# Kernel optimization log

Hardware: AMD Instinct MI355X
Metric: run time of the kernel (lower is better)

The kernel has to match this reference:

```python
import jax, jax.numpy as jnp
import numpy as np

NUM_ITERATIONS = 5
EPSILON_0 = 1.0
EPS = 1e-20


def setup_inputs() -> dict:
    key = jax.random.key(0)
    k1, k2 = jax.random.split(key)
    B, NIN, NOUT = 8192, 3072, 512
    x = jax.random.uniform(k1, (B, NIN), dtype=jnp.float32)
    w = jax.random.uniform(k2, (NOUT, NIN), dtype=jnp.float32)
    # weights setter normalizes rows to sum to 1
    w = w / w.sum(axis=1, keepdims=True)
    h_initial = jnp.full((NOUT,), 1.0 / NOUT, dtype=jnp.float32)
    return {"x": x, "weights": w, "h_initial": h_initial}


def reference(x, weights, h_initial):
    # x: [B, NIN], weights: [NOUT, NIN], h_initial: [NOUT]
    x = x / (x.sum(axis=1, keepdims=True) + EPS)  # input normalization in forward()
    B = x.shape[0]
    h = jnp.broadcast_to(h_initial[None, :], (B, h_initial.shape[0]))

    def step(h, _):
        # Original: h_w = h[:,:,None]*W[None]; h_w /= h_w.sum(1,keepdim)+eps;
        #           h_w = (h_w * x[:,None,:]).sum(-1)
        # Equivalent without materializing [B, NOUT, NIN]:
        denom = h @ weights                       # [B, NIN] = sum_n h_bn W_nk
        h_w = h * ((x / (denom + EPS)) @ weights.T)  # [B, NOUT]
        h_new = h + EPSILON_0 * h_w               # epsilon_0 > 0 branch
        h_new = h_new / (h_new.sum(axis=1, keepdims=True) + EPS)
        return h_new, None

    h, _ = jax.lax.scan(step, h, None, length=NUM_ITERATIONS)
    return h
```

## Files before the change

kernel.cpp:

```cpp
#include <hip/hip_runtime.h>


#define NIN 3072
#define NOUT 512

using f32x4 = __attribute__((ext_vector_type(4))) float;
using i32x8 = __attribute__((ext_vector_type(8))) int;

union frag32 { i32x8 v; uint4 q[2]; };

#define MFMA128(A, B, C) \
    __builtin_amdgcn_mfma_scale_f32_16x16x128_f8f6f4( \
        (A), (B), (C), 0, 0, 0, (int)0x7f7f7f7f, 0, (int)0x7f7f7f7f)

__device__ __forceinline__ unsigned short f2bf(float f) {
    unsigned int u = __builtin_bit_cast(unsigned int, f);
    return (unsigned short)((u + 0x7fffu + ((u >> 16) & 1u)) >> 16);
}
__device__ __forceinline__ float bf2f(unsigned short s) {
    unsigned int u = ((unsigned int)s) << 16;
    return __builtin_bit_cast(float, u);
}

#define LDS_BARRIER() do {                                   \
    asm volatile("s_waitcnt lgkmcnt(0)" ::: "memory");       \
    __builtin_amdgcn_s_barrier();                            \
    asm volatile("" ::: "memory");                           \
} while (0)

__global__ void prep_all(const float* __restrict__ x,
                         const float* __restrict__ W,
                         const float* __restrict__ h_init,
                         unsigned short* __restrict__ X2,
                         unsigned char* __restrict__ W1,
                         unsigned char* __restrict__ W2,
                         float* __restrict__ d0inv) {
    __shared__ float wsum[4];
    __shared__ float dred[8][32];
    const int bb = blockIdx.x;
    const int t  = threadIdx.x;

    if (bb < 8192) {
        const int b = bb;
        const float4* r4 = reinterpret_cast<const float4*>(x + (size_t)b * NIN);
        float s = 0.f;
        float4 v0 = r4[t], v1 = r4[t + 256], v2 = r4[t + 512];
        s = v0.x + v0.y + v0.z + v0.w + v1.x + v1.y + v1.z + v1.w + v2.x + v2.y + v2.z + v2.w;
        #pragma unroll
        for (int off = 32; off > 0; off >>= 1) s += __shfl_down(s, off, 64);
        int w = t >> 6, l = t & 63;
        if (l == 0) wsum[w] = s;
        __syncthreads();
        float inv = 16.0f / (wsum[0] + wsum[1] + wsum[2] + wsum[3] + 1e-20f);
        unsigned short* orow = X2 + (size_t)b * NIN;
        #pragma unroll
        for (int c = 0; c < 3; ++c) {
            float4 v = (c == 0) ? v0 : (c == 1) ? v1 : v2;
            ushort4 o;
            o.x = f2bf(v.x * inv); o.y = f2bf(v.y * inv);
            o.z = f2bf(v.z * inv); o.w = f2bf(v.w * inv);
            *reinterpret_cast<ushort4*>(orow + (t + c * 256) * 4) = o;
        }
    } else if (bb < 8192 + 384) {
        int tt = (bb - 8192) * 256 + t;
        unsigned int words[8];
        if (tt < 49152) {
            int l = tt & 63, g = tt >> 6;
            int s = g >> 5, rem = g & 31, w = rem >> 2, nt = rem & 3;
            int n = w * 64 + nt * 16 + (l & 15);
            int kbase = s * 128 + ((l >> 4) << 5);
            const float* src = W + (size_t)n * NIN + kbase;
            #pragma unroll
            for (int q = 0; q < 8; ++q) {
                float v0 = src[q * 4 + 0] * 4096.0f, v1 = src[q * 4 + 1] * 4096.0f;
                float v2 = src[q * 4 + 2] * 4096.0f, v3 = src[q * 4 + 3] * 4096.0f;
                int pk = __builtin_amdgcn_cvt_pk_fp8_f32(v0, v1, 0, false);
                pk     = __builtin_amdgcn_cvt_pk_fp8_f32(v2, v3, pk, true);
                words[q] = (unsigned int)pk;
            }
            uint4* dst = reinterpret_cast<uint4*>(W2 + (size_t)tt * 32);
            dst[0] = *reinterpret_cast<uint4*>(&words[0]);
            dst[1] = *reinterpret_cast<uint4*>(&words[4]);
        } else {
            int u = tt - 49152;
            int l = u & 63, g = u >> 6;
            int c = g & 3, sw = g >> 2;
            int w = sw & 7, s = sw >> 3;
            int kout = s * 128 + w * 16 + (l & 15);
            int nbase = c * 128 + ((l >> 4) << 5);
            #pragma unroll
            for (int q = 0; q < 8; ++q) {
                float v0 = W[(size_t)(nbase + q * 4 + 0) * NIN + kout] * 4096.0f;
                float v1 = W[(size_t)(nbase + q * 4 + 1) * NIN + kout] * 4096.0f;
                float v2 = W[(size_t)(nbase + q * 4 + 2) * NIN + kout] * 4096.0f;
                float v3 = W[(size_t)(nbase + q * 4 + 3) * NIN + kout] * 4096.0f;
                int pk = __builtin_amdgcn_cvt_pk_fp8_f32(v0, v1, 0, false);
                pk     = __builtin_amdgcn_cvt_pk_fp8_f32(v2, v3, pk, true);
                words[q] = (unsigned int)pk;
            }
            uint4* dst = reinterpret_cast<uint4*>(W1 + (size_t)u * 32);
            dst[0] = *reinterpret_cast<uint4*>(&words[0]);
            dst[1] = *reinterpret_cast<uint4*>(&words[4]);
        }
    } else {
        int kb = bb - 8576;
        int kid = t & 31, nsub = t >> 5;
        int k = kb * 32 + kid;
        int n0 = nsub * 64;
        float s = 0.f;
        const float* p = W + (size_t)n0 * NIN + k;
        #pragma unroll 8
        for (int n = 0; n < 64; ++n) s += h_init[n0 + n] * p[(size_t)n * NIN];
        dred[nsub][kid] = s;
        __syncthreads();
        if (t < 32) {
            float sm = 1e-20f;
            #pragma unroll
            for (int j = 0; j < 8; ++j) sm += dred[j][t];
            d0inv[kb * 32 + t] = 1.0f / sm;
        }
    }
}

__global__ __launch_bounds__(512, 1) void nnmf_main(
    const unsigned short* __restrict__ X2,
    const unsigned char* __restrict__ W1,
    const unsigned char* __restrict__ W2,
    const float* __restrict__ d0inv,
    const float* __restrict__ h_init,
    float* __restrict__ out)
{
    __shared__ unsigned char  h8_lds[32 * 528];
    __shared__ float          h32_lds[32 * 516];
    __shared__ unsigned short x_lds[32 * 136];
    __shared__ unsigned char  r8_lds[32 * 144];
    __shared__ float red[8][32];

    const int tid = threadIdx.x;
    const int w  = tid >> 6;
    const int l  = tid & 63;
    const int lo = l & 15;
    const int hi = l >> 4;
    const int b0 = blockIdx.x * 32;

    for (int idx = tid; idx < 32 * 512; idx += 512) {
        int r = idx >> 9, c = idx & 511;
        h32_lds[r * 516 + c] = h_init[c];
    }

    const int xrow = tid >> 4, xcc = tid & 15;
    const uint4* xg = reinterpret_cast<const uint4*>(X2 + (size_t)(b0 + xrow) * NIN + xcc * 8);
    unsigned short* xdst = &x_lds[xrow * 136 + xcc * 8];

    const unsigned char* w1base = W1 + (size_t)w * 8192 + (size_t)l * 32;
    const unsigned char* w2base = W2 + (size_t)w * 8192 + (size_t)l * 32;

    *reinterpret_cast<uint4*>(xdst) = xg[0];
    uint4 xnext = xg[16];
    frag32 w1buf[4];
    __syncthreads();

    const float DSCL = 9.5367431640625e-07f;
    const float TS   = 1.0f / 65536.0f;
    f32x4 tacc[2][4];

    for (int it = 0; it < 5; ++it) {
        #pragma unroll
        for (int m = 0; m < 2; ++m)
            #pragma unroll
            for (int nt = 0; nt < 4; ++nt)
                tacc[m][nt] = (f32x4){0.f, 0.f, 0.f, 0.f};

        for (int s = 0; s < 24; ++s) {
            const int sn  = (s + 1 == 24) ? 0 : s + 1;
            const int sn2 = (s + 2 >= 24) ? (s + 2 - 24) : s + 2;

            frag32 w2v[4];
            {
                const unsigned char* w2p = w2base + (size_t)s * 65536;
                #pragma unroll
                for (int nt = 0; nt < 4; ++nt) {
                    const uint4* p = reinterpret_cast<const uint4*>(w2p + nt * 2048);
                    w2v[nt].q[0] = p[0];
                    w2v[nt].q[1] = p[1];
                }
            }

            f32x4 d0 = {0,0,0,0}, d1 = {0,0,0,0};
            float dv = 0.f;
            if (it == 0) {
                dv = d0inv[s * 128 + w * 16 + lo];
            } else {
                #pragma unroll
                for (int c = 0; c < 4; ++c) {
                    frag32 ha0, ha1;
                    const uint4* p0 = reinterpret_cast<const uint4*>(
                        &h8_lds[lo * 528 + c * 128 + hi * 32]);
                    const uint4* p1 = reinterpret_cast<const uint4*>(
                        &h8_lds[(16 + lo) * 528 + c * 128 + hi * 32]);
                    ha0.q[0] = p0[0]; ha0.q[1] = p0[1];
                    ha1.q[0] = p1[0]; ha1.q[1] = p1[1];
                    d0 = MFMA128(ha0.v, w1buf[c].v, d0);
                    d1 = MFMA128(ha1.v, w1buf[c].v, d1);
                }
            }

            #pragma unroll
            for (int i = 0; i < 4; ++i) {
                int row0 = hi * 4 + i;
                float x0 = bf2f(x_lds[row0 * 136 + w * 16 + lo]);
                float x1 = bf2f(x_lds[(16 + row0) * 136 + w * 16 + lo]);
                float r0, r1;
                if (it == 0) { r0 = x0 * dv; r1 = x1 * dv; }
                else {
                    r0 = x0 * __builtin_amdgcn_rcpf(fmaf(d0[i], DSCL, 1e-20f));
                    r1 = x1 * __builtin_amdgcn_rcpf(fmaf(d1[i], DSCL, 1e-20f));
                }
                int c0 = __builtin_amdgcn_cvt_pk_fp8_f32(r0, r0, 0, false);
                int c1 = __builtin_amdgcn_cvt_pk_fp8_f32(r1, r1, 0, false);
                r8_lds[row0 * 144 + w * 16 + lo] = (unsigned char)(c0 & 0xff);
                r8_lds[(16 + row0) * 144 + w * 16 + lo] = (unsigned char)(c1 & 0xff);
            }
            LDS_BARRIER();

            frag32 ra0, ra1;
            {
                const uint4* p0 = reinterpret_cast<const uint4*>(&r8_lds[lo * 144 + hi * 32]);
                const uint4* p1 = reinterpret_cast<const uint4*>(&r8_lds[(16 + lo) * 144 + hi * 32]);
                ra0.q[0] = p0[0]; ra0.q[1] = p0[1];
                ra1.q[0] = p1[0]; ra1.q[1] = p1[1];
            }
            #pragma unroll
            for (int nt = 0; nt < 2; ++nt) {
                tacc[0][nt] = MFMA128(ra0.v, w2v[nt].v, tacc[0][nt]);
                tacc[1][nt] = MFMA128(ra1.v, w2v[nt].v, tacc[1][nt]);
            }

            if (it > 0 || s == 23) {
                const unsigned char* w1p = w1base + (size_t)sn * 65536;
                #pragma unroll
                for (int c = 0; c < 4; ++c) {
                    const uint4* p = reinterpret_cast<const uint4*>(w1p + c * 2048);
                    w1buf[c].q[0] = p[0];
                    w1buf[c].q[1] = p[1];
                }
            }

            #pragma unroll
            for (int nt = 2; nt < 4; ++nt) {
                tacc[0][nt] = MFMA128(ra0.v, w2v[nt].v, tacc[0][nt]);
                tacc[1][nt] = MFMA128(ra1.v, w2v[nt].v, tacc[1][nt]);
            }

            *reinterpret_cast<uint4*>(xdst) = xnext;
            xnext = xg[(size_t)sn2 * 16];
            LDS_BARRIER();
        }

        float hv_[2][4][4];
        float p[2][4];
        #pragma unroll
        for (int m = 0; m < 2; ++m)
            #pragma unroll
            for (int i = 0; i < 4; ++i) p[m][i] = 0.f;

        #pragma unroll
        for (int m = 0; m < 2; ++m)
            #pragma unroll
            for (int nt = 0; nt < 4; ++nt)
                #pragma unroll
                for (int i = 0; i < 4; ++i) {
                    int row = m * 16 + hi * 4 + i;
                    int col = w * 64 + nt * 16 + lo;
                    float hv = h32_lds[row * 516 + col];
                    float v = hv * (1.f + tacc[m][nt][i] * TS);
                    hv_[m][nt][i] = v;
                    p[m][i] += v;
                }
        #pragma unroll
        for (int mask = 1; mask < 16; mask <<= 1)
            #pragma unroll
            for (int m = 0; m < 2; ++m)
                #pragma unroll
                for (int i = 0; i < 4; ++i)
                    p[m][i] += __shfl_xor(p[m][i], mask, 64);
        if (lo == 0) {
            #pragma unroll
            for (int m = 0; m < 2; ++m)
                #pragma unroll
                for (int i = 0; i < 4; ++i)
                    red[w][m * 16 + hi * 4 + i] = p[m][i];
        }
        __syncthreads();
        float inv[2][4];
        #pragma unroll
        for (int m = 0; m < 2; ++m)
            #pragma unroll
            for (int i = 0; i < 4; ++i) {
                int row = m * 16 + hi * 4 + i;
                float S = 0.f;
                #pragma unroll
                for (int ww = 0; ww < 8; ++ww) S += red[ww][row];
                inv[m][i] = 1.f / (S + 1e-20f);
            }

        if (it < 4) {
            #pragma unroll
            for (int m = 0; m < 2; ++m)
                #pragma unroll
                for (int nt = 0; nt < 4; ++nt)
                    #pragma unroll
                    for (int i = 0; i < 4; ++i) {
                        int row = m * 16 + hi * 4 + i;
                        int col = w * 64 + nt * 16 + lo;
                        float hv = hv_[m][nt][i] * inv[m][i];
                        h32_lds[row * 516 + col] = hv;
                        int c = __builtin_amdgcn_cvt_pk_fp8_f32(hv * 256.0f, hv * 256.0f, 0, false);
                        h8_lds[row * 528 + col] = (unsigned char)(c & 0xff);
                    }
            __syncthreads();
        } else {
            #pragma unroll
            for (int m = 0; m < 2; ++m)
                #pragma unroll
                for (int nt = 0; nt < 4; ++nt)
                    #pragma unroll
                    for (int i = 0; i < 4; ++i) {
                        int row = m * 16 + hi * 4 + i;
                        int col = w * 64 + nt * 16 + lo;
                        out[(size_t)(b0 + row) * 512 + col] = hv_[m][nt][i] * inv[m][i];
                    }
        }
    }
}

extern "C" void kernel_launch(void* const* d_in, const int* in_sizes, int n_in,
                              void* d_out, int out_size, void* d_ws, size_t ws_size,
                              hipStream_t stream) {
    const float* x   = (const float*)d_in[0];
    const float* wgt = (const float*)d_in[1];
    const float* h0  = (const float*)d_in[2];
    float* out = (float*)d_out;

    unsigned short* X2 = (unsigned short*)d_ws;
    unsigned char*  W1 = (unsigned char*)((char*)d_ws + 50331648);
    unsigned char*  W2 = (unsigned char*)((char*)d_ws + 51904512);
    float* d0inv       = (float*)((char*)d_ws + 53477376);

    prep_all<<<8672, 256, 0, stream>>>(x, wgt, h0, X2, W1, W2, d0inv);
    nnmf_main<<<256, 512, 0, stream>>>(X2, W1, W2, d0inv, h0, out);
}
```

Measured before the change: 391.2 us.

## Double the K step per iteration to halve barriers and reuse h fragments

Widens the k-chunk processed per loop iteration from 128 to 256 columns, so each iteration runs 12 steps instead of 24. W1 and W2 are repacked in fp8 to match the new per-wave 32-column layout, and the x and r LDS tiles are widened to match. Each loaded h fragment now feeds two MFMAs, and the number of LDS barriers per iteration is halved. In exchange the kernel holds more weight fragments in registers and uses more LDS, which raises register pressure and could cause spills at 512 threads per block.

```diff
diff --git a/kernel.cpp b/kernel.cpp
--- a/kernel.cpp
+++ b/kernel.cpp
@@ -66,9 +66,11 @@
         unsigned int words[8];
         if (tt < 49152) {
             int l = tt & 63, g = tt >> 6;
-            int s = g >> 5, rem = g & 31, w = rem >> 2, nt = rem & 3;
+            int khalf = g & 1, q2 = g >> 1;
+            int nt = q2 & 3, q3 = q2 >> 2;
+            int w = q3 & 7, s = q3 >> 3;
             int n = w * 64 + nt * 16 + (l & 15);
-            int kbase = s * 128 + ((l >> 4) << 5);
+            int kbase = s * 256 + khalf * 128 + ((l >> 4) << 5);
             const float* src = W + (size_t)n * NIN + kbase;
             #pragma unroll
             for (int q = 0; q < 8; ++q) {
@@ -84,9 +86,10 @@
         } else {
             int u = tt - 49152;
             int l = u & 63, g = u >> 6;
-            int c = g & 3, sw = g >> 2;
-            int w = sw & 7, s = sw >> 3;
-            int kout = s * 128 + w * 16 + (l & 15);
+            int kt = g & 1, q2 = g >> 1;
+            int c = q2 & 3, q3 = q2 >> 2;
+            int w = q3 & 7, s = q3 >> 3;
+            int kout = s * 256 + w * 32 + kt * 16 + (l & 15);
             int nbase = c * 128 + ((l >> 4) << 5);
             #pragma unroll
             for (int q = 0; q < 8; ++q) {
@@ -132,8 +135,8 @@
 {
     __shared__ unsigned char  h8_lds[32 * 528];
     __shared__ float          h32_lds[32 * 516];
-    __shared__ unsigned short x_lds[32 * 136];
-    __shared__ unsigned char  r8_lds[32 * 144];
+    __shared__ unsigned short x_lds[32 * 264];
+    __shared__ unsigned char  r8_lds[32 * 272];
     __shared__ float red[8][32];
 
     const int tid = threadIdx.x;
@@ -149,15 +152,17 @@
     }
 
     const int xrow = tid >> 4, xcc = tid & 15;
-    const uint4* xg = reinterpret_cast<const uint4*>(X2 + (size_t)(b0 + xrow) * NIN + xcc * 8);
-    unsigned short* xdst = &x_lds[xrow * 136 + xcc * 8];
-
-    const unsigned char* w1base = W1 + (size_t)w * 8192 + (size_t)l * 32;
-    const unsigned char* w2base = W2 + (size_t)w * 8192 + (size_t)l * 32;
-
-    *reinterpret_cast<uint4*>(xdst) = xg[0];
-    uint4 xnext = xg[16];
-    frag32 w1buf[4];
+    const uint4* xgq = reinterpret_cast<const uint4*>(X2 + (size_t)(b0 + xrow) * NIN);
+    unsigned short* xdst0 = &x_lds[xrow * 264 + xcc * 8];
+    unsigned short* xdst1 = &x_lds[xrow * 264 + 128 + xcc * 8];
+
+    const unsigned char* w1base = W1 + (size_t)w * 16384 + (size_t)l * 32;
+    const unsigned char* w2base = W2 + (size_t)w * 16384 + (size_t)l * 32;
+
+    *reinterpret_cast<uint4*>(xdst0) = xgq[xcc];
+    *reinterpret_cast<uint4*>(xdst1) = xgq[xcc + 16];
+    uint4 xnA = xgq[32 + xcc], xnB = xgq[32 + xcc + 16];
+    frag32 w1w[6];
     __syncthreads();
 
     const float DSCL = 9.5367431640625e-07f;
@@ -171,89 +176,157 @@
             for (int nt = 0; nt < 4; ++nt)
                 tacc[m][nt] = (f32x4){0.f, 0.f, 0.f, 0.f};
 
-        for (int s = 0; s < 24; ++s) {
-            const int sn  = (s + 1 == 24) ? 0 : s + 1;
-            const int sn2 = (s + 2 >= 24) ? (s + 2 - 24) : s + 2;
-
-            frag32 w2v[4];
-            {
-                const unsigned char* w2p = w2base + (size_t)s * 65536;
-                #pragma unroll
-                for (int nt = 0; nt < 4; ++nt) {
-                    const uint4* p = reinterpret_cast<const uint4*>(w2p + nt * 2048);
-                    w2v[nt].q[0] = p[0];
-                    w2v[nt].q[1] = p[1];
-                }
-            }
-
-            f32x4 d0 = {0,0,0,0}, d1 = {0,0,0,0};
-            float dv = 0.f;
+        for (int s = 0; s < 12; ++s) {
+            const unsigned char* w1s = w1base + (size_t)s * 131072;
+            const unsigned char* w2s = w2base + (size_t)s * 131072;
+
+            f32x4 d00 = {0,0,0,0}, d01 = {0,0,0,0}, d10 = {0,0,0,0}, d11 = {0,0,0,0};
+            float dv0 = 0.f, dv1 = 0.f;
             if (it == 0) {
-                dv = d0inv[s * 128 + w * 16 + lo];
+                dv0 = d0inv[s * 256 + w * 32 + lo];
+                dv1 = d0inv[s * 256 + w * 32 + 16 + lo];
             } else {
-                #pragma unroll
-                for (int c = 0; c < 4; ++c) {
-                    frag32 ha0, ha1;
-                    const uint4* p0 = reinterpret_cast<const uint4*>(
-                        &h8_lds[lo * 528 + c * 128 + hi * 32]);
-                    const uint4* p1 = reinterpret_cast<const uint4*>(
-                        &h8_lds[(16 + lo) * 528 + c * 128 + hi * 32]);
+                frag32 ha0, ha1;
+                {
+                    const uint4* p0 = reinterpret_cast<const uint4*>(&h8_lds[lo * 528 + 0 * 128 + hi * 32]);
+                    const uint4* p1 = reinterpret_cast<const uint4*>(&h8_lds[(16 + lo) * 528 + 0 * 128 + hi * 32]);
                     ha0.q[0] = p0[0]; ha0.q[1] = p0[1];
                     ha1.q[0] = p1[0]; ha1.q[1] = p1[1];
-                    d0 = MFMA128(ha0.v, w1buf[c].v, d0);
-                    d1 = MFMA128(ha1.v, w1buf[c].v, d1);
-                }
-            }
-
-            #pragma unroll
-            for (int i = 0; i < 4; ++i) {
-                int row0 = hi * 4 + i;
-                float x0 = bf2f(x_lds[row0 * 136 + w * 16 + lo]);
-                float x1 = bf2f(x_lds[(16 + row0) * 136 + w * 16 + lo]);
-                float r0, r1;
-                if (it == 0) { r0 = x0 * dv; r1 = x1 * dv; }
-                else {
-                    r0 = x0 * __builtin_amdgcn_rcpf(fmaf(d0[i], DSCL, 1e-20f));
-                    r1 = x1 * __builtin_amdgcn_rcpf(fmaf(d1[i], DSCL, 1e-20f));
-                }
-                int c0 = __builtin_amdgcn_cvt_pk_fp8_f32(r0, r0, 0, false);
-                int c1 = __builtin_amdgcn_cvt_pk_fp8_f32(r1, r1, 0, false);
-                r8_lds[row0 * 144 + w * 16 + lo] = (unsigned char)(c0 & 0xff);
-                r8_lds[(16 + row0) * 144 + w * 16 + lo] = (unsigned char)(c1 & 0xff);
+                    d00 = MFMA128(ha0.v, w1w[0].v, d00);
+                    d01 = MFMA128(ha0.v, w1w[1].v, d01);
+                    d10 = MFMA128(ha1.v, w1w[0].v, d10);
+                    d11 = MFMA128(ha1.v, w1w[1].v, d11);
+                }
+                {
+                    const uint4* pa = reinterpret_cast<const uint4*>(w1s + 4 * 2048);
+                    const uint4* pb = reinterpret_cast<const uint4*>(w1s + 5 * 2048);
+                    w1w[4].q[0] = pa[0]; w1w[4].q[1] = pa[1];
+                    w1w[5].q[0] = pb[0]; w1w[5].q[1] = pb[1];
+                }
+                {
+                    const uint4* p0 = reinterpret_cast<const uint4*>(&h8_lds[lo * 528 + 1 * 128 + hi * 32]);
+                    const uint4* p1 = reinterpret_cast<const uint4*>(&h8_lds[(16 + lo) * 528 + 1 * 128 + hi * 32]);
+                    ha0.q[0] = p0[0]; ha0.q[1] = p0[1];
+                    ha1.q[0] = p1[0]; ha1.q[1] = p1[1];
+                    d00 = MFMA128(ha0.v, w1w[2].v, d00);
+                    d01 = MFMA128(ha0.v, w1w[3].v, d01);
+                    d10 = MFMA128(ha1.v, w1w[2].v, d10);
+                    d11 = MFMA128(ha1.v, w1w[3].v, d11);
+                }
+                {
+                    const uint4* pa = reinterpret_cast<const uint4*>(w1s + 6 * 2048);
+                    const uint4* pb = reinterpret_cast<const uint4*>(w1s + 7 * 2048);
+                    w1w[0].q[0] = pa[0]; w1w[0].q[1] = pa[1];
+                    w1w[1].q[0] = pb[0]; w1w[1].q[1] = pb[1];
+                }
+                {
+                    const uint4* p0 = reinterpret_cast<const uint4*>(&h8_lds[lo * 528 + 2 * 128 + hi * 32]);
+                    const uint4* p1 = reinterpret_cast<const uint4*>(&h8_lds[(16 + lo) * 528 + 2 * 128 + hi * 32]);
+                    ha0.q[0] = p0[0]; ha0.q[1] = p0[1];
+                    ha1.q[0] = p1[0]; ha1.q[1] = p1[1];
+                    d00 = MFMA128(ha0.v, w1w[4].v, d00);
+                    d01 = MFMA128(ha0.v, w1w[5].v, d01);
+                    d10 = MFMA128(ha1.v, w1w[4].v, d10);
+                    d11 = MFMA128(ha1.v, w1w[5].v, d11);
+                }
+                {
+                    const uint4* p0 = reinterpret_cast<const uint4*>(&h8_lds[lo * 528 + 3 * 128 + hi * 32]);
+                    const uint4* p1 = reinterpret_cast<const uint4*>(&h8_lds[(16 + lo) * 528 + 3 * 128 + hi * 32]);
+                    ha0.q[0] = p0[0]; ha0.q[1] = p0[1];
+                    ha1.q[0] = p1[0]; ha1.q[1] = p1[1];
+                    d00 = MFMA128(ha0.v, w1w[0].v, d00);
+                    d01 = MFMA128(ha0.v, w1w[1].v, d01);
+                    d10 = MFMA128(ha1.v, w1w[0].v, d10);
+                    d11 = MFMA128(ha1.v, w1w[1].v, d11);
+                }
+            }
+
+            frag32 w2a[4];
+            #pragma unroll
+            for (int nt = 0; nt < 4; ++nt) {
+                const uint4* p = reinterpret_cast<const uint4*>(w2s + (nt * 2) * 2048);
+                w2a[nt].q[0] = p[0];
+                w2a[nt].q[1] = p[1];
+            }
+
+            #pragma unroll
+            for (int kt = 0; kt < 2; ++kt) {
+                int col = w * 32 + kt * 16 + lo;
+                #pragma unroll
+                for (int i = 0; i < 4; ++i) {
+                    int row0 = hi * 4 + i;
+                    float x0 = bf2f(x_lds[row0 * 264 + col]);
+                    float x1 = bf2f(x_lds[(16 + row0) * 264 + col]);
+                    float r0, r1;
+                    if (it == 0) {
+                        float dvv = kt ? dv1 : dv0;
+                        r0 = x0 * dvv; r1 = x1 * dvv;
+                    } else {
+                        float e0 = kt ? d01[i] : d00[i];
+                        float e1 = kt ? d11[i] : d10[i];
+                        r0 = x0 * __builtin_amdgcn_rcpf(fmaf(e0, DSCL, 1e-20f));
+                        r1 = x1 * __builtin_amdgcn_rcpf(fmaf(e1, DSCL, 1e-20f));
+                    }
+                    int c0 = __builtin_amdgcn_cvt_pk_fp8_f32(r0, r0, 0, false);
+                    int c1 = __builtin_amdgcn_cvt_pk_fp8_f32(r1, r1, 0, false);
+                    r8_lds[row0 * 272 + col] = (unsigned char)(c0 & 0xff);
+                    r8_lds[(16 + row0) * 272 + col] = (unsigned char)(c1 & 0xff);
+                }
             }
             LDS_BARRIER();
 
-            frag32 ra0, ra1;
+            frag32 w2b[4];
+            #pragma unroll
+            for (int nt = 0; nt < 4; ++nt) {
+                const uint4* p = reinterpret_cast<const uint4*>(w2s + (nt * 2 + 1) * 2048);
+                w2b[nt].q[0] = p[0];
+                w2b[nt].q[1] = p[1];
+            }
+
             {
-                const uint4* p0 = reinterpret_cast<const uint4*>(&r8_lds[lo * 144 + hi * 32]);
-                const uint4* p1 = reinterpret_cast<const uint4*>(&r8_lds[(16 + lo) * 144 + hi * 32]);
+                frag32 ra0, ra1;
+                const uint4* p0 = reinterpret_cast<const uint4*>(&r8_lds[lo * 272 + hi * 32]);
+                const uint4* p1 = reinterpret_cast<const uint4*>(&r8_lds[(16 + lo) * 272 + hi * 32]);
                 ra0.q[0] = p0[0]; ra0.q[1] = p0[1];
                 ra1.q[0] = p1[0]; ra1.q[1] = p1[1];
-            }
-            #pragma unroll
-            for (int nt = 0; nt < 2; ++nt) {
-                tacc[0][nt] = MFMA128(ra0.v, w2v[nt].v, tacc[0][nt]);
-                tacc[1][nt] = MFMA128(ra1.v, w2v[nt].v, tacc[1][nt]);
-            }
-
-            if (it > 0 || s == 23) {
-                const unsigned char* w1p = w1base + (size_t)sn * 65536;
-                #pragma unroll
-                for (int c = 0; c < 4; ++c) {
-                    const uint4* p = reinterpret_cast<const uint4*>(w1p + c * 2048);
-                    w1buf[c].q[0] = p[0];
-                    w1buf[c].q[1] = p[1];
-                }
-            }
-
-            #pragma unroll
-            for (int nt = 2; nt < 4; ++nt) {
-                tacc[0][nt] = MFMA128(ra0.v, w2v[nt].v, tacc[0][nt]);
-                tacc[1][nt] = MFMA128(ra1.v, w2v[nt].v, tacc[1][nt]);
-            }
-
-            *reinterpret_cast<uint4*>(xdst) = xnext;
-            xnext = xg[(size_t)sn2 * 16];
+                #pragma unroll
+                for (int nt = 0; nt < 4; ++nt) {
+                    tacc[0][nt] = MFMA128(ra0.v, w2a[nt].v, tacc[0][nt]);
+                    tacc[1][nt] = MFMA128(ra1.v, w2a[nt].v, tacc[1][nt]);
+                }
+            }
+
+            if (it > 0 || s == 11) {
+                int sw = (s == 11) ? 0 : s + 1;
+                const unsigned char* w1p = w1base + (size_t)sw * 131072;
+                #pragma unroll
+                for (int f = 0; f < 4; ++f) {
+                    const uint4* p = reinterpret_cast<const uint4*>(w1p + f * 2048);
+                    w1w[f].q[0] = p[0];
+                    w1w[f].q[1] = p[1];
+                }
+            }
+
+            {
+                frag32 ra0, ra1;
+                const uint4* p0 = reinterpret_cast<const uint4*>(&r8_lds[lo * 272 + 128 + hi * 32]);
+                const uint4* p1 = reinterpret_cast<const uint4*>(&r8_lds[(16 + lo) * 272 + 128 + hi * 32]);
+                ra0.q[0] = p0[0]; ra0.q[1] = p0[1];
+                ra1.q[0] = p1[0]; ra1.q[1] = p1[1];
+                #pragma unroll
+                for (int nt = 0; nt < 4; ++nt) {
+                    tacc[0][nt] = MFMA128(ra0.v, w2b[nt].v, tacc[0][nt]);
+                    tacc[1][nt] = MFMA128(ra1.v, w2b[nt].v, tacc[1][nt]);
+                }
+            }
+
+            *reinterpret_cast<uint4*>(xdst0) = xnA;
+            *reinterpret_cast<uint4*>(xdst1) = xnB;
+            {
+                int f = s + 2; if (f >= 12) f -= 12;
+                xnA = xgq[(size_t)f * 32 + xcc];
+                xnB = xgq[(size_t)f * 32 + xcc + 16];
+            }
             LDS_BARRIER();
         }
 
```

After: 402.4 us. +2.9%, slower.
